# Kernel optimization log

Measured on AMD Instinct MI355X. Metric: run time of the kernel, lower is better.

## Reference

```python
import jax, jax.numpy as jnp
import numpy as np

B, S, E = 4, 2048, 1024
H = 16
D = E // H  # head_dim = 64


def setup_inputs() -> dict:
    key = jax.random.key(0)
    k1, k2, k3 = jax.random.split(key, 3)
    scale_qkv = 1.0 / np.sqrt(E)
    return {
        "x": jax.random.normal(k1, (B, S, E), dtype=jnp.float32),
        "Wqkv": jax.random.normal(k2, (E, 3 * E), dtype=jnp.float32) * scale_qkv,
        "bqkv": jnp.zeros((3 * E,), dtype=jnp.float32),
        "Wproj": jax.random.normal(k3, (E, E), dtype=jnp.float32) * scale_qkv,
        "bproj": jnp.zeros((E,), dtype=jnp.float32),
    }


def reference(x, Wqkv, bqkv, Wproj, bproj):
    b, s, e = x.shape
    qkv = x @ Wqkv + bqkv                      # [B,S,3E]
    q, k, v = jnp.split(qkv, 3, axis=-1)
    # [B,S,E] -> [B,H,S,D]
    q = q.reshape(b, s, H, D).transpose(0, 2, 1, 3)
    k = k.reshape(b, s, H, D).transpose(0, 2, 1, 3)
    v = v.reshape(b, s, H, D).transpose(0, 2, 1, 3)
    scores = jnp.einsum('bhqd,bhkd->bhqk', q, k) * (D ** -0.5)  # [B,H,S,S]
    causal = jnp.tril(jnp.ones((s, s), dtype=bool))
    scores = jnp.where(causal, scores, -jnp.inf)
    weights = jax.nn.softmax(scores, axis=-1)  # dropout p=0 -> identity
    out = jnp.einsum('bhqk,bhkd->bhqd', weights, v)  # [B,H,S,D]
    out = out.transpose(0, 2, 1, 3).reshape(b, s, e)
    return out @ Wproj + bproj
```

## Files before the change

kernel.cpp:

```cpp
#include <hip/hip_runtime.h>
#include <hip/hip_bf16.h>
#include <stdint.h>

#define B_ 4
#define S_ 2048
#define E_ 1024
#define H_ 16
#define D_ 64
#define M_ 8192
#define N1_ 3072
#define QSCALE 0.18033688011112042f

typedef __attribute__((ext_vector_type(8))) short bf16x8;
typedef __attribute__((ext_vector_type(4))) float f32x4;
typedef __attribute__((ext_vector_type(16))) float f32x16;
typedef __attribute__((ext_vector_type(4))) short short4v;

__device__ __forceinline__ short f2b(float f) {
  union { float f; unsigned u; } c; c.f = f;
  unsigned u = c.u + 0x7fffu + ((c.u >> 16) & 1u);
  return (short)(u >> 16);
}

__device__ __forceinline__ float fexp2(float x) {
#if __has_builtin(__builtin_amdgcn_exp2f)
  return __builtin_amdgcn_exp2f(x);
#else
  return exp2f(x);
#endif
}

__device__ __forceinline__ unsigned cvtpk(float lo, float hi2) {
  unsigned r;
  asm("v_cvt_pk_bf16_f32 %0, %1, %2" : "=v"(r) : "v"(lo), "v"(hi2));
  return r;
}

__device__ __forceinline__ void gload16(const void* g, void* l) {
  __builtin_amdgcn_global_load_lds((const __attribute__((address_space(1))) void*)g,
                                   (__attribute__((address_space(3))) void*)l, 16, 0, 0);
}

__global__ void conv_kernel(const float* __restrict__ in, short* __restrict__ out) {
  int idx = blockIdx.x * 256 + threadIdx.x;
  const float4* p = (const float4*)in;
  float4 a = p[(size_t)idx * 2];
  float4 b = p[(size_t)idx * 2 + 1];
  bf16x8 v;
  v[0] = f2b(a.x); v[1] = f2b(a.y); v[2] = f2b(a.z); v[3] = f2b(a.w);
  v[4] = f2b(b.x); v[5] = f2b(b.y); v[6] = f2b(b.z); v[7] = f2b(b.w);
  *(bf16x8*)(out + (size_t)idx * 8) = v;
}

__global__ void trans_kernel(const float* __restrict__ in, short* __restrict__ out,
                             int K, int N) {
  __shared__ float tile[32][33];
  int n0 = blockIdx.x * 32, k0 = blockIdx.y * 32;
  int tx = threadIdx.x & 31, ty = threadIdx.x >> 5;
  #pragma unroll
  for (int i = 0; i < 4; ++i)
    tile[ty + i * 8][tx] = in[(size_t)(k0 + ty + i * 8) * N + n0 + tx];
  __syncthreads();
  #pragma unroll
  for (int i = 0; i < 4; ++i)
    out[(size_t)(n0 + ty + i * 8) * K + k0 + tx] = f2b(tile[tx][ty + i * 8]);
}

template<bool SCATTER>
__global__ __launch_bounds__(256)
void gemm_kernel(const short* __restrict__ A, const short* __restrict__ Bt,
                 const float* __restrict__ bias,
                 short* __restrict__ oQ, short* __restrict__ oK, short* __restrict__ oV,
                 float* __restrict__ oC, int Kdim, int Ndim)
{
  __shared__ short Asub[128 * 64];
  __shared__ short Bsub[128 * 64];
  const int tid = threadIdx.x;
  const int l = tid & 63, w = tid >> 6;
  const int wr = w >> 1, wc = w & 1;
  const int lr = l & 15, lg = l >> 4;

  const int nwg = gridDim.x * gridDim.y;
  const int lin = blockIdx.y * gridDim.x + blockIdx.x;
  const int lin2 = (lin & 7) * (nwg >> 3) + (lin >> 3);
  const int m0 = (lin2 / gridDim.x) * 128, n0 = (lin2 % gridDim.x) * 128;

  const int srow = w * 8 + (l >> 3);
  const int scol = ((l & 7) ^ (l >> 3)) << 3;

  f32x4 acc[4][4] = {};

  for (int k0 = 0; k0 < Kdim; k0 += 64) {
    __syncthreads();
    #pragma unroll
    for (int i = 0; i < 4; ++i) {
      gload16(A  + (size_t)(m0 + i * 32 + srow) * Kdim + k0 + scol,
              (char*)Asub + (i * 32 + w * 8) * 128);
      gload16(Bt + (size_t)(n0 + i * 32 + srow) * Kdim + k0 + scol,
              (char*)Bsub + (i * 32 + w * 8) * 128);
    }
    __syncthreads();
    #pragma unroll
    for (int kk = 0; kk < 64; kk += 32) {
      bf16x8 af[4], bfr[4];
      const int ce2 = (kk + lg * 8) << 1;
      #pragma unroll
      for (int mi = 0; mi < 4; ++mi) {
        int rr = wr * 64 + mi * 16 + lr;
        af[mi] = *(const bf16x8*)((const char*)Asub + rr * 128 + (ce2 ^ ((rr & 7) << 4)));
      }
      #pragma unroll
      for (int ni = 0; ni < 4; ++ni) {
        int rr = wc * 64 + ni * 16 + lr;
        bfr[ni] = *(const bf16x8*)((const char*)Bsub + rr * 128 + (ce2 ^ ((rr & 7) << 4)));
      }
      __builtin_amdgcn_s_setprio(1);
      #pragma unroll
      for (int mi = 0; mi < 4; ++mi)
        #pragma unroll
        for (int ni = 0; ni < 4; ++ni)
          acc[mi][ni] = __builtin_amdgcn_mfma_f32_16x16x32_bf16(af[mi], bfr[ni], acc[mi][ni], 0, 0, 0);
      __builtin_amdgcn_s_setprio(0);
    }
  }

  #pragma unroll
  for (int mi = 0; mi < 4; ++mi) {
    #pragma unroll
    for (int ni = 0; ni < 4; ++ni) {
      const int row0 = m0 + wr * 64 + mi * 16 + lg * 4;
      const int col  = n0 + wc * 64 + ni * 16 + lr;
      const float bv = bias[col];
      if constexpr (SCATTER) {
        const int which = col >> 10;
        const int e = col & 1023;
        const int h = e >> 6, d = e & 63;
        const int b = row0 >> 11, s = row0 & 2047;
        if (which == 2) {
          short4v pv;
          #pragma unroll
          for (int r = 0; r < 4; ++r) pv[r] = f2b(acc[mi][ni][r] + bv);
          *(short4v*)(oV + ((size_t)((b * H_ + h) * D_ + d)) * S_ + s) = pv;
        } else {
          short* dst = which ? oK : oQ;
          const float sc = which ? 1.0f : QSCALE;
          #pragma unroll
          for (int r = 0; r < 4; ++r)
            dst[((size_t)((b * H_ + h) * S_ + s + r)) * D_ + d] = f2b((acc[mi][ni][r] + bv) * sc);
        }
      } else {
        #pragma unroll
        for (int r = 0; r < 4; ++r)
          oC[(size_t)(row0 + r) * Ndim + col] = acc[mi][ni][r] + bv;
      }
    }
  }
}

__global__ __launch_bounds__(512)
void attn_kernel(const short* __restrict__ Q, const short* __restrict__ K,
                 const short* __restrict__ vT, short* __restrict__ O)
{
  __shared__ short Kl[4][64 * 64];
  __shared__ short Vl[4][64 * 64];

  const int qt = (S_ / 128 - 1) - (blockIdx.x >> 6);
  const int bh = blockIdx.x & 63;
  const int tid = threadIdx.x, l = tid & 63, w = tid >> 6;
  const int qw = w & 3, g = w >> 2;
  const int lc = l & 31, hi = l >> 5;
  const int sl8 = l >> 3;
  const int scol = 8 * ((l & 7) ^ sl8);

  const short* Qb = Q  + (size_t)bh * (S_ * D_);
  const short* Kb = K  + (size_t)bh * (S_ * D_);
  const short* Vg = vT + (size_t)bh * (S_ * D_);

  const int q0w = qt * 128 + qw * 32;
  const int ktL = (q0w + 31) >> 6;
  const int NT2 = qt + 1;

  bf16x8 qr[4];
  #pragma unroll
  for (int ds = 0; ds < 4; ++ds)
    qr[ds] = *(const bf16x8*)(Qb + (size_t)(q0w + lc) * D_ + ds * 16 + hi * 8);

  f32x16 accA{}, accB{};
  float lsum = 0.f;

  auto stage = [&](int slot, int kt2) {
    short* kl = &Kl[slot][(qw * 8) * 64];
    short* vl = &Vl[slot][(qw * 8) * 64];
    const size_t kr = (size_t)(kt2 * 64 + qw * 8 + sl8);
    gload16(Kb + kr * 64 + scol, kl);
    gload16(Kb + (kr + 32) * 64 + scol, kl + 32 * 64);
    const size_t vr = (size_t)(qw * 8 + sl8);
    gload16(Vg + vr * S_ + kt2 * 64 + scol, vl);
    gload16(Vg + (vr + 32) * S_ + kt2 * 64 + scol, vl + 32 * 64);
  };

  stage(g * 2, g);
  __syncthreads();

  for (int i = 0; i < NT2; ++i) {
    const int kt = 2 * i + g;
    const int slot = g * 2 + (i & 1);
    if (i + 1 < NT2) stage(g * 2 + ((i & 1) ^ 1), kt + 2);

    if (kt <= ktL) {
      const char* Kc = (const char*)Kl[slot];
      const char* Vc = (const char*)Vl[slot];
      const int rsw = (lc & 7) << 4;
      f32x16 s0{}, s1{};
      __builtin_amdgcn_s_setprio(1);
      #pragma unroll
      for (int ds = 0; ds < 4; ++ds) {
        const int byt = ds * 32 + hi * 16;
        bf16x8 a0 = *(const bf16x8*)(Kc + lc * 128 + (byt ^ rsw));
        bf16x8 a1 = *(const bf16x8*)(Kc + (32 + lc) * 128 + (byt ^ rsw));
        s0 = __builtin_amdgcn_mfma_f32_32x32x16_bf16(a0, qr[ds], s0, 0, 0, 0);
        s1 = __builtin_amdgcn_mfma_f32_32x32x16_bf16(a1, qr[ds], s1, 0, 0, 0);
      }
      __builtin_amdgcn_s_setprio(0);
      float p[32];
      #pragma unroll
      for (int r = 0; r < 16; ++r) { p[r] = s0[r]; p[16 + r] = s1[r]; }
      if (kt == ktL) {
        const int qq = q0w + lc - kt * 64;
        #pragma unroll
        for (int r = 0; r < 16; ++r) {
          const int k0 = (r & 3) + 8 * (r >> 2) + 4 * hi;
          if (k0 > qq)      p[r]      = -1e30f;
          if (k0 + 32 > qq) p[16 + r] = -1e30f;
        }
      }
      float rs0 = 0.f, rs1 = 0.f, rs2 = 0.f, rs3 = 0.f;
      #pragma unroll
      for (int r = 0; r < 8; ++r) {
        p[r]      = fexp2(p[r]);      rs0 += p[r];
        p[8 + r]  = fexp2(p[8 + r]);  rs1 += p[8 + r];
        p[16 + r] = fexp2(p[16 + r]); rs2 += p[16 + r];
        p[24 + r] = fexp2(p[24 + r]); rs3 += p[24 + r];
      }
      float rs = (rs0 + rs1) + (rs2 + rs3);
      rs += __shfl_xor(rs, 32);
      lsum += rs;
      #pragma unroll
      for (int ks = 0; ks < 4; ++ks) {
        const int b8 = ks * 8;
        const unsigned A0 = cvtpk(p[b8 + 0], p[b8 + 1]);
        const unsigned A1 = cvtpk(p[b8 + 2], p[b8 + 3]);
        const unsigned B0 = cvtpk(p[b8 + 4], p[b8 + 5]);
        const unsigned B1 = cvtpk(p[b8 + 6], p[b8 + 7]);
        const unsigned u0 = __shfl_xor(hi ? A0 : B0, 32);
        const unsigned u1 = __shfl_xor(hi ? A1 : B1, 32);
        union { unsigned u[4]; bf16x8 v; } W;
        W.u[0] = hi ? u0 : A0;
        W.u[1] = hi ? u1 : A1;
        W.u[2] = hi ? B0 : u0;
        W.u[3] = hi ? B1 : u1;
        const int byt = ks * 32 + hi * 16;
        bf16x8 va = *(const bf16x8*)(Vc + lc * 128 + (byt ^ rsw));
        bf16x8 vb = *(const bf16x8*)(Vc + (32 + lc) * 128 + (byt ^ rsw));
        __builtin_amdgcn_s_setprio(1);
        accA = __builtin_amdgcn_mfma_f32_32x32x16_bf16(va, W.v, accA, 0, 0, 0);
        accB = __builtin_amdgcn_mfma_f32_32x32x16_bf16(vb, W.v, accB, 0, 0, 0);
        __builtin_amdgcn_s_setprio(0);
      }
    }
    __syncthreads();
  }

  float* accsA = (float*)Kl;
  float* accsB = (float*)Vl;
  float* stats = (float*)((char*)Kl + 20480);
  const int mi = qw * 64 + l;
  if (g == 1) {
    #pragma unroll
    for (int r = 0; r < 16; ++r) {
      accsA[mi * 17 + r] = accA[r];
      accsB[mi * 17 + r] = accB[r];
    }
    stats[mi] = lsum;
  }
  __syncthreads();
  if (g == 0) {
    const float rl = 1.0f / (lsum + stats[mi]);
    const int h = bh & 15, b = bh >> 4;
    short* Ob = O + ((size_t)(b * S_ + q0w + lc)) * E_ + h * 64;
    #pragma unroll
    for (int gq = 0; gq < 4; ++gq) {
      short4v o0, o1;
      #pragma unroll
      for (int i = 0; i < 4; ++i) {
        o0[i] = f2b((accA[4 * gq + i] + accsA[mi * 17 + 4 * gq + i]) * rl);
        o1[i] = f2b((accB[4 * gq + i] + accsB[mi * 17 + 4 * gq + i]) * rl);
      }
      *(short4v*)(Ob + 8 * gq + 4 * hi) = o0;
      *(short4v*)(Ob + 32 + 8 * gq + 4 * hi) = o1;
    }
  }
}

extern "C" void kernel_launch(void* const* d_in, const int* in_sizes, int n_in,
                              void* d_out, int out_size, void* d_ws, size_t ws_size,
                              hipStream_t stream)
{
  const float* x     = (const float*)d_in[0];
  const float* Wqkv  = (const float*)d_in[1];
  const float* bqkv  = (const float*)d_in[2];
  const float* Wproj = (const float*)d_in[3];
  const float* bproj = (const float*)d_in[4];
  float* out = (float*)d_out;

  char* ws = (char*)d_ws;
  short* xb     = (short*)(ws + (size_t)0);
  short* wqkvT  = (short*)(ws + (size_t)16 * 1024 * 1024);
  short* wprojT = (short*)(ws + (size_t)22 * 1024 * 1024);
  short* qb     = (short*)(ws + (size_t)24 * 1024 * 1024);
  short* kb     = (short*)(ws + (size_t)40 * 1024 * 1024);
  short* vb     = (short*)(ws + (size_t)56 * 1024 * 1024);
  short* ob     = (short*)(ws + (size_t)72 * 1024 * 1024);

  conv_kernel<<<4096, 256, 0, stream>>>(x, xb);
  trans_kernel<<<dim3(N1_ / 32, E_ / 32), 256, 0, stream>>>(Wqkv, wqkvT, E_, N1_);
  trans_kernel<<<dim3(E_ / 32, E_ / 32), 256, 0, stream>>>(Wproj, wprojT, E_, E_);
  gemm_kernel<true><<<dim3(N1_ / 128, M_ / 128), 256, 0, stream>>>(
      xb, wqkvT, bqkv, qb, kb, vb, nullptr, E_, N1_);
  attn_kernel<<<(S_ / 128) * (B_ * H_), 512, 0, stream>>>(qb, kb, vb, ob);
  gemm_kernel<false><<<dim3(E_ / 128, M_ / 128), 256, 0, stream>>>(
      ob, wprojT, bproj, nullptr, nullptr, nullptr, out, E_, E_);
}
```

Baseline: 165.6 us.

## Load K/V tiles directly from global into registers, drop LDS staging

Replaces the double-buffered LDS staging of K and V tiles with per-wave direct global loads into registers, and removes the per-iteration block barriers. Each wave now loops only over its active key tiles. This gives up the data reuse that shared staging provided across the four query waves, so each wave fetches K/V separately through cache. It also drops the synchronisation and the LDS traffic.

```diff
diff --git a/kernel.cpp b/kernel.cpp
--- a/kernel.cpp
+++ b/kernel.cpp
@@ -161,16 +161,15 @@
 void attn_kernel(const short* __restrict__ Q, const short* __restrict__ K,
                  const short* __restrict__ vT, short* __restrict__ O)
 {
-  __shared__ short Kl[4][64 * 64];
-  __shared__ short Vl[4][64 * 64];
+  __shared__ float accsA[256 * 17];
+  __shared__ float accsB[256 * 17];
+  __shared__ float stats[256];
 
   const int qt = (S_ / 128 - 1) - (blockIdx.x >> 6);
   const int bh = blockIdx.x & 63;
   const int tid = threadIdx.x, l = tid & 63, w = tid >> 6;
   const int qw = w & 3, g = w >> 2;
   const int lc = l & 31, hi = l >> 5;
-  const int sl8 = l >> 3;
-  const int scol = 8 * ((l & 7) ^ sl8);
 
   const short* Qb = Q  + (size_t)bh * (S_ * D_);
   const short* Kb = K  + (size_t)bh * (S_ * D_);
@@ -178,7 +177,7 @@
 
   const int q0w = qt * 128 + qw * 32;
   const int ktL = (q0w + 31) >> 6;
-  const int NT2 = qt + 1;
+  const int nAct = (ktL < g) ? 0 : ((ktL - g) >> 1) + 1;
 
   bf16x8 qr[4];
   #pragma unroll
@@ -188,92 +187,74 @@
   f32x16 accA{}, accB{};
   float lsum = 0.f;
 
-  auto stage = [&](int slot, int kt2) {
-    short* kl = &Kl[slot][(qw * 8) * 64];
-    short* vl = &Vl[slot][(qw * 8) * 64];
-    const size_t kr = (size_t)(kt2 * 64 + qw * 8 + sl8);
-    gload16(Kb + kr * 64 + scol, kl);
-    gload16(Kb + (kr + 32) * 64 + scol, kl + 32 * 64);
-    const size_t vr = (size_t)(qw * 8 + sl8);
-    gload16(Vg + vr * S_ + kt2 * 64 + scol, vl);
-    gload16(Vg + (vr + 32) * S_ + kt2 * 64 + scol, vl + 32 * 64);
-  };
-
-  stage(g * 2, g);
-  __syncthreads();
-
-  for (int i = 0; i < NT2; ++i) {
+  for (int i = 0; i < nAct; ++i) {
     const int kt = 2 * i + g;
-    const int slot = g * 2 + (i & 1);
-    if (i + 1 < NT2) stage(g * 2 + ((i & 1) ^ 1), kt + 2);
-
-    if (kt <= ktL) {
-      const char* Kc = (const char*)Kl[slot];
-      const char* Vc = (const char*)Vl[slot];
-      const int rsw = (lc & 7) << 4;
-      f32x16 s0{}, s1{};
+    const short* Kr = Kb + (size_t)(kt * 64 + lc) * D_ + hi * 8;
+    bf16x8 ka[4], kb2[4];
+    #pragma unroll
+    for (int ds = 0; ds < 4; ++ds) {
+      ka[ds]  = *(const bf16x8*)(Kr + ds * 16);
+      kb2[ds] = *(const bf16x8*)(Kr + 32 * D_ + ds * 16);
+    }
+    f32x16 s0{}, s1{};
+    __builtin_amdgcn_s_setprio(1);
+    #pragma unroll
+    for (int ds = 0; ds < 4; ++ds) {
+      s0 = __builtin_amdgcn_mfma_f32_32x32x16_bf16(ka[ds],  qr[ds], s0, 0, 0, 0);
+      s1 = __builtin_amdgcn_mfma_f32_32x32x16_bf16(kb2[ds], qr[ds], s1, 0, 0, 0);
+    }
+    __builtin_amdgcn_s_setprio(0);
+    const short* Vr = Vg + (size_t)lc * S_ + kt * 64 + hi * 8;
+    bf16x8 va[4], vb2[4];
+    #pragma unroll
+    for (int ks = 0; ks < 4; ++ks) {
+      va[ks]  = *(const bf16x8*)(Vr + ks * 16);
+      vb2[ks] = *(const bf16x8*)(Vr + 32 * S_ + ks * 16);
+    }
+    float p[32];
+    #pragma unroll
+    for (int r = 0; r < 16; ++r) { p[r] = s0[r]; p[16 + r] = s1[r]; }
+    if (kt == ktL) {
+      const int qq = q0w + lc - kt * 64;
+      #pragma unroll
+      for (int r = 0; r < 16; ++r) {
+        const int k0 = (r & 3) + 8 * (r >> 2) + 4 * hi;
+        if (k0 > qq)      p[r]      = -1e30f;
+        if (k0 + 32 > qq) p[16 + r] = -1e30f;
+      }
+    }
+    float rs0 = 0.f, rs1 = 0.f, rs2 = 0.f, rs3 = 0.f;
+    #pragma unroll
+    for (int r = 0; r < 8; ++r) {
+      p[r]      = fexp2(p[r]);      rs0 += p[r];
+      p[8 + r]  = fexp2(p[8 + r]);  rs1 += p[8 + r];
+      p[16 + r] = fexp2(p[16 + r]); rs2 += p[16 + r];
+      p[24 + r] = fexp2(p[24 + r]); rs3 += p[24 + r];
+    }
+    float rs = (rs0 + rs1) + (rs2 + rs3);
+    rs += __shfl_xor(rs, 32);
+    lsum += rs;
+    #pragma unroll
+    for (int ks = 0; ks < 4; ++ks) {
+      const int b8 = ks * 8;
+      const unsigned A0 = cvtpk(p[b8 + 0], p[b8 + 1]);
+      const unsigned A1 = cvtpk(p[b8 + 2], p[b8 + 3]);
+      const unsigned B0 = cvtpk(p[b8 + 4], p[b8 + 5]);
+      const unsigned B1 = cvtpk(p[b8 + 6], p[b8 + 7]);
+      const unsigned u0 = __shfl_xor(hi ? A0 : B0, 32);
+      const unsigned u1 = __shfl_xor(hi ? A1 : B1, 32);
+      union { unsigned u[4]; bf16x8 v; } W;
+      W.u[0] = hi ? u0 : A0;
+      W.u[1] = hi ? u1 : A1;
+      W.u[2] = hi ? B0 : u0;
+      W.u[3] = hi ? B1 : u1;
       __builtin_amdgcn_s_setprio(1);
-      #pragma unroll
-      for (int ds = 0; ds < 4; ++ds) {
-        const int byt = ds * 32 + hi * 16;
-        bf16x8 a0 = *(const bf16x8*)(Kc + lc * 128 + (byt ^ rsw));
-        bf16x8 a1 = *(const bf16x8*)(Kc + (32 + lc) * 128 + (byt ^ rsw));
-        s0 = __builtin_amdgcn_mfma_f32_32x32x16_bf16(a0, qr[ds], s0, 0, 0, 0);
-        s1 = __builtin_amdgcn_mfma_f32_32x32x16_bf16(a1, qr[ds], s1, 0, 0, 0);
-      }
+      accA = __builtin_amdgcn_mfma_f32_32x32x16_bf16(va[ks],  W.v, accA, 0, 0, 0);
+      accB = __builtin_amdgcn_mfma_f32_32x32x16_bf16(vb2[ks], W.v, accB, 0, 0, 0);
       __builtin_amdgcn_s_setprio(0);
-      float p[32];
-      #pragma unroll
-      for (int r = 0; r < 16; ++r) { p[r] = s0[r]; p[16 + r] = s1[r]; }
-      if (kt == ktL) {
-        const int qq = q0w + lc - kt * 64;
-        #pragma unroll
-        for (int r = 0; r < 16; ++r) {
-          const int k0 = (r & 3) + 8 * (r >> 2) + 4 * hi;
-          if (k0 > qq)      p[r]      = -1e30f;
-          if (k0 + 32 > qq) p[16 + r] = -1e30f;
-        }
-      }
-      float rs0 = 0.f, rs1 = 0.f, rs2 = 0.f, rs3 = 0.f;
-      #pragma unroll
-      for (int r = 0; r < 8; ++r) {
-        p[r]      = fexp2(p[r]);      rs0 += p[r];
-        p[8 + r]  = fexp2(p[8 + r]);  rs1 += p[8 + r];
-        p[16 + r] = fexp2(p[16 + r]); rs2 += p[16 + r];
-        p[24 + r] = fexp2(p[24 + r]); rs3 += p[24 + r];
-      }
-      float rs = (rs0 + rs1) + (rs2 + rs3);
-      rs += __shfl_xor(rs, 32);
-      lsum += rs;
-      #pragma unroll
-      for (int ks = 0; ks < 4; ++ks) {
-        const int b8 = ks * 8;
-        const unsigned A0 = cvtpk(p[b8 + 0], p[b8 + 1]);
-        const unsigned A1 = cvtpk(p[b8 + 2], p[b8 + 3]);
-        const unsigned B0 = cvtpk(p[b8 + 4], p[b8 + 5]);
-        const unsigned B1 = cvtpk(p[b8 + 6], p[b8 + 7]);
-        const unsigned u0 = __shfl_xor(hi ? A0 : B0, 32);
-        const unsigned u1 = __shfl_xor(hi ? A1 : B1, 32);
-        union { unsigned u[4]; bf16x8 v; } W;
-        W.u[0] = hi ? u0 : A0;
-        W.u[1] = hi ? u1 : A1;
-        W.u[2] = hi ? B0 : u0;
-        W.u[3] = hi ? B1 : u1;
-        const int byt = ks * 32 + hi * 16;
-        bf16x8 va = *(const bf16x8*)(Vc + lc * 128 + (byt ^ rsw));
-        bf16x8 vb = *(const bf16x8*)(Vc + (32 + lc) * 128 + (byt ^ rsw));
-        __builtin_amdgcn_s_setprio(1);
-        accA = __builtin_amdgcn_mfma_f32_32x32x16_bf16(va, W.v, accA, 0, 0, 0);
-        accB = __builtin_amdgcn_mfma_f32_32x32x16_bf16(vb, W.v, accB, 0, 0, 0);
-        __builtin_amdgcn_s_setprio(0);
-      }
-    }
-    __syncthreads();
-  }
-
-  float* accsA = (float*)Kl;
-  float* accsB = (float*)Vl;
-  float* stats = (float*)((char*)Kl + 20480);
+    }
+  }
+
   const int mi = qw * 64 + l;
   if (g == 1) {
     #pragma unroll
```

Measured after the change: 243.9 us. 1.47x slower.

## Drop split-K wave groups in attention; use 256-thread blocks walking all key tiles

Applied to the files above, without the earlier changes.

The attention kernel previously used 8 waves per block, with two groups each processing alternate key tiles into separate LDS slots and combining partial accumulators and row sums through shared memory at the end. It now uses 4 waves per block that walk every key tile sequentially with a single double-buffered K/V stage. This removes the final LDS reduction and barrier and halves LDS per block so more blocks can be resident. In exchange each wave does twice as many serial iterations, which halves intra-block parallelism over keys and lengthens the per-block critical path.

```diff
diff --git a/kernel.cpp b/kernel.cpp
--- a/kernel.cpp
+++ b/kernel.cpp
@@ -157,17 +157,16 @@
   }
 }
 
-__global__ __launch_bounds__(512)
+__global__ __launch_bounds__(256, 4)
 void attn_kernel(const short* __restrict__ Q, const short* __restrict__ K,
                  const short* __restrict__ vT, short* __restrict__ O)
 {
-  __shared__ short Kl[4][64 * 64];
-  __shared__ short Vl[4][64 * 64];
+  __shared__ short Kl[2][64 * 64];
+  __shared__ short Vl[2][64 * 64];
 
   const int qt = (S_ / 128 - 1) - (blockIdx.x >> 6);
   const int bh = blockIdx.x & 63;
   const int tid = threadIdx.x, l = tid & 63, w = tid >> 6;
-  const int qw = w & 3, g = w >> 2;
   const int lc = l & 31, hi = l >> 5;
   const int sl8 = l >> 3;
   const int scol = 8 * ((l & 7) ^ sl8);
@@ -176,9 +175,9 @@
   const short* Kb = K  + (size_t)bh * (S_ * D_);
   const short* Vg = vT + (size_t)bh * (S_ * D_);
 
-  const int q0w = qt * 128 + qw * 32;
+  const int q0w = qt * 128 + w * 32;
   const int ktL = (q0w + 31) >> 6;
-  const int NT2 = qt + 1;
+  const int NTB = 2 * qt + 2;
 
   bf16x8 qr[4];
   #pragma unroll
@@ -187,30 +186,29 @@
 
   f32x16 accA{}, accB{};
   float lsum = 0.f;
-
-  auto stage = [&](int slot, int kt2) {
-    short* kl = &Kl[slot][(qw * 8) * 64];
-    short* vl = &Vl[slot][(qw * 8) * 64];
-    const size_t kr = (size_t)(kt2 * 64 + qw * 8 + sl8);
+  const int rsw = (lc & 7) << 4;
+
+  auto stage = [&](int buf, int kt2) {
+    short* kl = &Kl[buf][(w * 16) * 64];
+    short* vl = &Vl[buf][(w * 16) * 64];
+    const size_t kr = (size_t)(kt2 * 64 + w * 16 + sl8);
     gload16(Kb + kr * 64 + scol, kl);
-    gload16(Kb + (kr + 32) * 64 + scol, kl + 32 * 64);
-    const size_t vr = (size_t)(qw * 8 + sl8);
+    gload16(Kb + (kr + 8) * 64 + scol, kl + 8 * 64);
+    const size_t vr = (size_t)(w * 16 + sl8);
     gload16(Vg + vr * S_ + kt2 * 64 + scol, vl);
-    gload16(Vg + (vr + 32) * S_ + kt2 * 64 + scol, vl + 32 * 64);
+    gload16(Vg + (vr + 8) * S_ + kt2 * 64 + scol, vl + 8 * 64);
   };
 
-  stage(g * 2, g);
+  stage(0, 0);
   __syncthreads();
 
-  for (int i = 0; i < NT2; ++i) {
-    const int kt = 2 * i + g;
-    const int slot = g * 2 + (i & 1);
-    if (i + 1 < NT2) stage(g * 2 + ((i & 1) ^ 1), kt + 2);
+  for (int kt = 0; kt < NTB; ++kt) {
+    const int cur = kt & 1;
+    if (kt + 1 < NTB) stage(cur ^ 1, kt + 1);
 
     if (kt <= ktL) {
-      const char* Kc = (const char*)Kl[slot];
-      const char* Vc = (const char*)Vl[slot];
-      const int rsw = (lc & 7) << 4;
+      const char* Kc = (const char*)Kl[cur];
+      const char* Vc = (const char*)Vl[cur];
       f32x16 s0{}, s1{};
       __builtin_amdgcn_s_setprio(1);
       #pragma unroll
@@ -271,34 +269,19 @@
     __syncthreads();
   }
 
-  float* accsA = (float*)Kl;
-  float* accsB = (float*)Vl;
-  float* stats = (float*)((char*)Kl + 20480);
-  const int mi = qw * 64 + l;
-  if (g == 1) {
+  const float rl = 1.0f / lsum;
+  const int h = bh & 15, b = bh >> 4;
+  short* Ob = O + ((size_t)(b * S_ + q0w + lc)) * E_ + h * 64;
+  #pragma unroll
+  for (int gq = 0; gq < 4; ++gq) {
+    short4v o0, o1;
     #pragma unroll
-    for (int r = 0; r < 16; ++r) {
-      accsA[mi * 17 + r] = accA[r];
-      accsB[mi * 17 + r] = accB[r];
-    }
-    stats[mi] = lsum;
-  }
-  __syncthreads();
-  if (g == 0) {
-    const float rl = 1.0f / (lsum + stats[mi]);
-    const int h = bh & 15, b = bh >> 4;
-    short* Ob = O + ((size_t)(b * S_ + q0w + lc)) * E_ + h * 64;
-    #pragma unroll
-    for (int gq = 0; gq < 4; ++gq) {
-      short4v o0, o1;
-      #pragma unroll
-      for (int i = 0; i < 4; ++i) {
-        o0[i] = f2b((accA[4 * gq + i] + accsA[mi * 17 + 4 * gq + i]) * rl);
-        o1[i] = f2b((accB[4 * gq + i] + accsB[mi * 17 + 4 * gq + i]) * rl);
-      }
-      *(short4v*)(Ob + 8 * gq + 4 * hi) = o0;
-      *(short4v*)(Ob + 32 + 8 * gq + 4 * hi) = o1;
-    }
+    for (int i = 0; i < 4; ++i) {
+      o0[i] = f2b(accA[4 * gq + i] * rl);
+      o1[i] = f2b(accB[4 * gq + i] * rl);
+    }
+    *(short4v*)(Ob + 8 * gq + 4 * hi) = o0;
+    *(short4v*)(Ob + 32 + 8 * gq + 4 * hi) = o1;
   }
 }
 
@@ -327,7 +310,7 @@
   trans_kernel<<<dim3(E_ / 32, E_ / 32), 256, 0, stream>>>(Wproj, wprojT, E_, E_);
   gemm_kernel<true><<<dim3(N1_ / 128, M_ / 128), 256, 0, stream>>>(
       xb, wqkvT, bqkv, qb, kb, vb, nullptr, E_, N1_);
-  attn_kernel<<<(S_ / 128) * (B_ * H_), 512, 0, stream>>>(qb, kb, vb, ob);
+  attn_kernel<<<(S_ / 128) * (B_ * H_), 256, 0, stream>>>(qb, kb, vb, ob);
   gemm_kernel<false><<<dim3(E_ / 128, M_ / 128), 256, 0, stream>>>(
       ob, wprojT, bproj, nullptr, nullptr, nullptr, out, E_, E_);
 }
```

Result: no change. 164.2 us (-0.9%).
